# Performance work log

Measured on AMD Instinct MI355X. Metric: run time of the kernel, lower is better.

Reference implementation:

```python
import jax, jax.numpy as jnp
import numpy as np

D_MODEL, D_K, D_V = 1024, 64, 64
B, S = 4, 4096


def setup_inputs() -> dict:
    key = jax.random.key(0)
    ks = jax.random.split(key, 13)
    s = 1.0 / np.sqrt(D_MODEL)
    inp = {
        "q": jax.random.normal(ks[0], (B, S, D_MODEL), jnp.float32),
        "k": jax.random.normal(ks[1], (B, S, D_MODEL), jnp.float32),
        "v": jax.random.normal(ks[2], (B, S, D_MODEL), jnp.float32),
        "mask": jax.random.randint(ks[3], (1, S, S), 0, 2, jnp.int32),
        "Wq": jax.random.normal(ks[4], (D_K, D_MODEL), jnp.float32) * s,
        "bq": jax.random.normal(ks[5], (D_K,), jnp.float32) * s,
        "Wk": jax.random.normal(ks[6], (D_K, D_MODEL), jnp.float32) * s,
        "bk": jax.random.normal(ks[7], (D_K,), jnp.float32) * s,
        "Wv": jax.random.normal(ks[8], (D_V, D_MODEL), jnp.float32) * s,
        "bv": jax.random.normal(ks[9], (D_V,), jnp.float32) * s,
        "Wo": jax.random.normal(ks[10], (D_MODEL, D_V), jnp.float32) / np.sqrt(D_V),
        "bo": jax.random.normal(ks[11], (D_MODEL,), jnp.float32) / np.sqrt(D_V),
    }
    return inp


def reference(q, k, v, mask, Wq, bq, Wk, bk, Wv, bv, Wo, bo):
    # linear projections (torch Linear: x @ W.T + b)
    qh = jnp.einsum("bsd,kd->bsk", q, Wq) + bq   # [B,S,d_k]
    kh = jnp.einsum("bsd,kd->bsk", k, Wk) + bk   # [B,S,d_k]
    vh = jnp.einsum("bsd,vd->bsv", v, Wv) + bv   # [B,S,d_v]
    scale = 1.0 / jnp.sqrt(jnp.float32(D_K))
    scores = jnp.einsum("bqk,bmk->bqm", qh, kh) * scale  # [B,S,S]
    scores = jnp.where(mask == 0, jnp.float32(-1e9), scores)
    attn = jax.nn.softmax(scores, axis=-1)
    out = jnp.einsum("bqm,bmv->bqv", attn, vh)   # [B,S,d_v]
    return jnp.einsum("bqv,dv->bqd", out, Wo) + bo
```

## Files before the change

### kernel.cpp

```cpp
#include <hip/hip_runtime.h>
#include <cmath>

typedef __attribute__((ext_vector_type(8))) short bf16x8;
typedef __attribute__((ext_vector_type(4))) short bf16x4;
typedef __attribute__((ext_vector_type(4))) float f32x4;
typedef unsigned int u32;
typedef __attribute__((address_space(1))) const u32 gu32;
typedef __attribute__((address_space(3))) u32 lu32;

constexpr int B_ = 4;
constexpr int S_ = 4096;
constexpr int DM_ = 1024;
constexpr int DK_ = 64;
constexpr int NROW = B_ * S_;

__device__ __forceinline__ short f2bf(float x) {
  union { float f; unsigned u; } c; c.f = x;
  unsigned r = (c.u + 0x7FFF + ((c.u >> 16) & 1)) >> 16;
  return (short)r;
}
__device__ __forceinline__ float bf2f(short h) {
  union { float f; unsigned u; } c; c.u = ((unsigned)(unsigned short)h) << 16;
  return c.f;
}
__device__ __forceinline__ void gl16(const void* g, void* l) {
  __builtin_amdgcn_global_load_lds((gu32*)g, (lu32*)l, 16, 0, 0);
}

__global__ __launch_bounds__(256) void prep(
    const int* __restrict__ mask, unsigned long long* __restrict__ bits,
    const float* __restrict__ Wq, const float* __restrict__ Wk,
    const float* __restrict__ Wv, short* __restrict__ wbf) {
  if (blockIdx.x < 1024) {
    const int wid = (blockIdx.x * 256 + threadIdx.x) >> 6;
    const int lane = threadIdx.x & 63;
    const size_t base = (size_t)wid * 4096;
    for (int it = 0; it < 64; ++it) {
      int m = mask[base + it * 64 + lane];
      unsigned long long b = __ballot(m != 0);
      if (lane == 0) bits[(size_t)wid * 64 + it] = b;
    }
  } else {
    const int mat = blockIdx.x - 1024;
    const float* W = mat == 0 ? Wq : (mat == 1 ? Wk : Wv);
    short* dst = wbf + (size_t)mat * DK_ * DM_;
    const int t = threadIdx.x;
#pragma unroll 4
    for (int i = 0; i < 32; ++i) {
      int idx = i * 2048 + t * 8;
      f32x4 a0 = *(const f32x4*)(W + idx);
      f32x4 a1 = *(const f32x4*)(W + idx + 4);
      bf16x8 h;
#pragma unroll
      for (int j = 0; j < 4; ++j) { h[j] = f2bf(a0[j]); h[j + 4] = f2bf(a1[j]); }
      *(bf16x8*)(dst + idx) = h;
    }
  }
}

__global__ __launch_bounds__(256) void proj_mfma(
    const float* __restrict__ q, const float* __restrict__ k,
    const float* __restrict__ v, const short* __restrict__ wbf,
    const float* __restrict__ bq, const float* __restrict__ bk,
    const float* __restrict__ bv,
    short* __restrict__ qh, short* __restrict__ kh, short* __restrict__ vhT) {
  __shared__ __align__(16) char smem[49152];

  const int mat = blockIdx.z;
  const char* Xb = (const char*)(mat == 0 ? q : (mat == 1 ? k : v));
  const char* Wb = (const char*)(wbf + (size_t)mat * DK_ * DM_);
  const float* bias = mat == 0 ? bq : (mat == 1 ? bk : bv);

  const int t = threadIdx.x;
  const int row0 = blockIdx.x * 64;
  const int lane = t & 63, w = t >> 6, quad = lane >> 4, l16 = lane & 15;

  f32x4 acc[4] = {};

  auto stage = [&](int buf, int ks) {
    const int k0 = ks * 64;
#pragma unroll
    for (int i = 0; i < 4; ++i) {
      int o = t * 16 + i * 4096;
      int row = o >> 8, col = o & 255;
      int scol = col ^ ((row & 7) << 4);
      gl16(Xb + (size_t)(row0 + row) * (DM_ * 4) + k0 * 4 + scol,
           smem + buf * 16384 + o);
    }
#pragma unroll
    for (int i = 0; i < 2; ++i) {
      int o = t * 16 + i * 4096;
      int row = o >> 7, col = o & 127;
      int scol = col ^ ((row & 7) << 4);
      gl16(Wb + row * 2048 + k0 * 2 + scol,
           smem + 32768 + buf * 8192 + o);
    }
  };

  auto compute = [&](int buf) {
    const char* xs = smem + buf * 16384;
    const char* ws = smem + 32768 + buf * 8192;
    const int xrow = 16 * w + l16;
    const int xsw = (xrow & 7) << 4;
#pragma unroll
    for (int c = 0; c < 2; ++c) {
      bf16x8 bw[4];
#pragma unroll
      for (int ct = 0; ct < 4; ++ct) {
        int wr = 16 * ct + l16;
        bw[ct] = *(const bf16x8*)(ws + wr * 128 +
                                  ((c * 64 + quad * 16) ^ ((wr & 7) << 4)));
      }
      int xb = xrow * 256 + ((c * 128 + quad * 32) ^ xsw);
      f32x4 x0 = *(const f32x4*)(xs + xb);
      f32x4 x1 = *(const f32x4*)(xs + (xb ^ 16));
      bf16x8 ahi, alo;
#pragma unroll
      for (int j = 0; j < 4; ++j) {
        short h0 = f2bf(x0[j]); ahi[j] = h0;     alo[j]     = f2bf(x0[j] - bf2f(h0));
        short h1 = f2bf(x1[j]); ahi[j + 4] = h1; alo[j + 4] = f2bf(x1[j] - bf2f(h1));
      }
#pragma unroll
      for (int ct = 0; ct < 4; ++ct) {
        acc[ct] = __builtin_amdgcn_mfma_f32_16x16x32_bf16(ahi, bw[ct], acc[ct], 0, 0, 0);
        acc[ct] = __builtin_amdgcn_mfma_f32_16x16x32_bf16(alo, bw[ct], acc[ct], 0, 0, 0);
      }
    }
  };

  stage(0, 0);
  __syncthreads();
  int cur = 0;
#pragma unroll 1
  for (int ks = 0; ks < 16; ++ks) {
    if (ks < 15) stage(cur ^ 1, ks + 1);
    compute(cur);
    __syncthreads();
    cur ^= 1;
  }

  float bs[4];
#pragma unroll
  for (int ct = 0; ct < 4; ++ct) bs[ct] = bias[16 * ct + l16];

  short* dstq = (mat == 0) ? qh : kh;
#pragma unroll
  for (int ct = 0; ct < 4; ++ct)
#pragma unroll
    for (int reg = 0; reg < 4; ++reg) {
      int r = row0 + 16 * w + quad * 4 + reg;
      int c = 16 * ct + l16;
      short hv = f2bf(acc[ct][reg] + bs[ct]);
      if (mat == 2)
        vhT[((size_t)(r >> 12) * DK_ + c) * S_ + (r & 4095)] = hv;
      else
        dstq[(size_t)r * DK_ + c] = hv;
    }
}

__global__ __launch_bounds__(256) void attn_mfma(
    const short* __restrict__ qh, const short* __restrict__ kh,
    const short* __restrict__ vhT, const unsigned int* __restrict__ mbits,
    float* __restrict__ Opart, float* __restrict__ mpart,
    float* __restrict__ lpart, int ns) {
  __shared__ short ks[64][72];
  __shared__ short vt[64][72];
  __shared__ short ps[4][16][72];

  const int b = blockIdx.z;
  const int split = blockIdx.y;
  const int q0 = blockIdx.x * 64;
  const int t = threadIdx.x, lane = t & 63, w = t >> 6;
  const int quad = lane >> 4, l16 = lane & 15;
  const int myq = q0 + 16 * w + l16;

  const int kt0 = split * (S_ / ns);
  const int kt1 = kt0 + S_ / ns;

  bf16x8 qf[2];
  {
    const short* src = qh + ((size_t)b * S_ + myq) * DK_ + quad * 8;
    qf[0] = *(const bf16x8*)src;
    qf[1] = *(const bf16x8*)(src + 32);
  }

  f32x4 ao[4] = {};
  float m_i = -INFINITY, l_i = 0.0f;

  const int sr = t >> 2;
  const int sseg = t & 3;

  for (int kt = kt0; kt < kt1; kt += 64) {
    __syncthreads();
    {
      const short* srck = kh + ((size_t)b * S_ + kt + sr) * DK_;
      *(bf16x8*)&ks[sr][8 * sseg]       = *(const bf16x8*)(srck + 8 * sseg);
      *(bf16x8*)&ks[sr][8 * (sseg + 4)] = *(const bf16x8*)(srck + 8 * (sseg + 4));
      const short* srcv = vhT + ((size_t)b * DK_ + sr) * S_ + kt;
      *(bf16x8*)&vt[sr][8 * sseg]       = *(const bf16x8*)(srcv + 8 * sseg);
      *(bf16x8*)&vt[sr][8 * (sseg + 4)] = *(const bf16x8*)(srcv + 8 * (sseg + 4));
    }
    const uint2 mw = *(const uint2*)&mbits[(size_t)myq * 128 + (kt >> 5)];
    __syncthreads();

    f32x4 sacc[4] = {};
#pragma unroll
    for (int c = 0; c < 2; ++c)
#pragma unroll
      for (int tt = 0; tt < 4; ++tt) {
        bf16x8 a = *(const bf16x8*)&ks[16 * tt + l16][c * 32 + quad * 8];
        sacc[tt] = __builtin_amdgcn_mfma_f32_16x16x32_bf16(a, qf[c], sacc[tt], 0, 0, 0);
      }

    float sc[16];
#pragma unroll
    for (int tt = 0; tt < 4; ++tt) {
      unsigned wrd = (tt & 2) ? mw.y : mw.x;
      int base = (tt & 1) * 16 + quad * 4;
#pragma unroll
      for (int r = 0; r < 4; ++r)
        sc[tt * 4 + r] = ((wrd >> (base + r)) & 1) ? sacc[tt][r] * 0.125f : -1e9f;
    }

    float mx = sc[0];
#pragma unroll
    for (int i = 1; i < 16; ++i) mx = fmaxf(mx, sc[i]);
    mx = fmaxf(mx, __shfl_xor(mx, 16));
    mx = fmaxf(mx, __shfl_xor(mx, 32));
    float m_new = fmaxf(m_i, mx);
    float alpha = __expf(m_i - m_new);
    float p[16], sum = 0.0f;
#pragma unroll
    for (int i = 0; i < 16; ++i) { p[i] = __expf(sc[i] - m_new); sum += p[i]; }
    sum += __shfl_xor(sum, 16);
    sum += __shfl_xor(sum, 32);
    l_i = l_i * alpha + sum;
    m_i = m_new;

#pragma unroll
    for (int tt = 0; tt < 4; ++tt) {
      bf16x4 pk;
#pragma unroll
      for (int r = 0; r < 4; ++r) pk[r] = f2bf(p[tt * 4 + r]);
      *(bf16x4*)&ps[w][l16][16 * tt + quad * 4] = pk;
    }

#pragma unroll
    for (int dt = 0; dt < 4; ++dt)
#pragma unroll
      for (int r = 0; r < 4; ++r) ao[dt][r] *= alpha;

#pragma unroll
    for (int c = 0; c < 2; ++c) {
      bf16x8 bp = *(const bf16x8*)&ps[w][l16][c * 32 + quad * 8];
#pragma unroll
      for (int dt = 0; dt < 4; ++dt) {
        bf16x8 av = *(const bf16x8*)&vt[16 * dt + l16][c * 32 + quad * 8];
        ao[dt] = __builtin_amdgcn_mfma_f32_16x16x32_bf16(av, bp, ao[dt], 0, 0, 0);
      }
    }
  }

  const size_t prow = (size_t)split * NROW + (size_t)b * S_ + myq;
#pragma unroll
  for (int dt = 0; dt < 4; ++dt)
    *(f32x4*)&Opart[prow * DK_ + 16 * dt + quad * 4] = ao[dt];
  if (quad == 0) {
    mpart[prow] = m_i;
    lpart[prow] = l_i;
  }
}

__global__ __launch_bounds__(256) void attn_combine(
    const float* __restrict__ Opart, const float* __restrict__ mpart,
    const float* __restrict__ lpart, short* __restrict__ o_bf, int ns) {
  const int t = threadIdx.x;
  const int row = blockIdx.x * 64 + (t >> 2);
  const int c0 = (t & 3) * 16;

  float M = -INFINITY;
  for (int s = 0; s < ns; ++s) M = fmaxf(M, mpart[(size_t)s * NROW + row]);
  float L = 0.0f, wt[4];
  for (int s = 0; s < ns; ++s) {
    wt[s] = __expf(mpart[(size_t)s * NROW + row] - M);
    L += wt[s] * lpart[(size_t)s * NROW + row];
  }
  float acc[16] = {};
  for (int s = 0; s < ns; ++s) {
    const float* src = Opart + ((size_t)s * NROW + row) * DK_ + c0;
#pragma unroll
    for (int j = 0; j < 16; j += 4) {
      f32x4 vv = *(const f32x4*)(src + j);
#pragma unroll
      for (int r = 0; r < 4; ++r) acc[j + r] += wt[s] * vv[r];
    }
  }
  const float inv = 1.0f / L;
  bf16x8 o0, o1;
#pragma unroll
  for (int j = 0; j < 8; ++j) {
    o0[j] = f2bf(acc[j] * inv);
    o1[j] = f2bf(acc[j + 8] * inv);
  }
  *(bf16x8*)&o_bf[(size_t)row * DK_ + c0]     = o0;
  *(bf16x8*)&o_bf[(size_t)row * DK_ + c0 + 8] = o1;
}

__global__ __launch_bounds__(256) void outproj_mfma(
    const short* __restrict__ o_bf, const float* __restrict__ Wo,
    const float* __restrict__ bo, float* __restrict__ out) {
  __shared__ short os[64][72];
  __shared__ short wos[256][72];

  const int t = threadIdx.x, lane = t & 63, w = t >> 6;
  const int quad = lane >> 4, l16 = lane & 15;
  const int s0 = blockIdx.y * 64;
  const int dm0 = blockIdx.x * 256;

  {
    int r = t >> 2, cq = (t & 3) * 16;
    const short* src = o_bf + (size_t)(s0 + r) * DK_ + cq;
    *(bf16x8*)&os[r][cq]     = *(const bf16x8*)src;
    *(bf16x8*)&os[r][cq + 8] = *(const bf16x8*)(src + 8);
  }
#pragma unroll
  for (int pass = 0; pass < 4; ++pass) {
    int r = pass * 64 + (t >> 2), cq = (t & 3) * 16;
    const float* src = Wo + (size_t)(dm0 + r) * DK_ + cq;
    f32x4 a0 = *(const f32x4*)src, a1 = *(const f32x4*)(src + 4);
    f32x4 a2 = *(const f32x4*)(src + 8), a3 = *(const f32x4*)(src + 12);
    bf16x8 v0, v1;
#pragma unroll
    for (int j = 0; j < 4; ++j) {
      v0[j] = f2bf(a0[j]); v0[j + 4] = f2bf(a1[j]);
      v1[j] = f2bf(a2[j]); v1[j + 4] = f2bf(a3[j]);
    }
    *(bf16x8*)&wos[r][cq]     = v0;
    *(bf16x8*)&wos[r][cq + 8] = v1;
  }
  __syncthreads();

  bf16x8 af[2];
#pragma unroll
  for (int c = 0; c < 2; ++c)
    af[c] = *(const bf16x8*)&os[16 * w + l16][c * 32 + quad * 8];

  f32x4 acc[16] = {};
#pragma unroll
  for (int c = 0; c < 2; ++c)
#pragma unroll
    for (int nt = 0; nt < 16; ++nt) {
      bf16x8 bw = *(const bf16x8*)&wos[16 * nt + l16][c * 32 + quad * 8];
      acc[nt] = __builtin_amdgcn_mfma_f32_16x16x32_bf16(af[c], bw, acc[nt], 0, 0, 0);
    }

  float bias_r[16];
#pragma unroll
  for (int nt = 0; nt < 16; ++nt) bias_r[nt] = bo[dm0 + 16 * nt + l16];

#pragma unroll
  for (int nt = 0; nt < 16; ++nt)
#pragma unroll
    for (int reg = 0; reg < 4; ++reg) {
      int s = s0 + 16 * w + quad * 4 + reg;
      int dm = dm0 + 16 * nt + l16;
      out[(size_t)s * DM_ + dm] = acc[nt][reg] + bias_r[nt];
    }
}

extern "C" void kernel_launch(void* const* d_in, const int* in_sizes, int n_in,
                              void* d_out, int out_size, void* d_ws,
                              size_t ws_size, hipStream_t stream) {
  (void)in_sizes; (void)n_in; (void)out_size;
  const float* q  = (const float*)d_in[0];
  const float* k  = (const float*)d_in[1];
  const float* v  = (const float*)d_in[2];
  const int* mask = (const int*)d_in[3];
  const float* Wq = (const float*)d_in[4];
  const float* bq = (const float*)d_in[5];
  const float* Wk = (const float*)d_in[6];
  const float* bk = (const float*)d_in[7];
  const float* Wv = (const float*)d_in[8];
  const float* bv = (const float*)d_in[9];
  const float* Wo = (const float*)d_in[10];
  const float* bo = (const float*)d_in[11];
  float* out = (float*)d_out;

  short* qh  = (short*)d_ws;
  short* kh  = qh + (size_t)NROW * DK_;
  short* vhT = kh + (size_t)NROW * DK_;
  unsigned int* mbits = (unsigned int*)(vhT + (size_t)NROW * DK_);
  short* o_bf = (short*)(mbits + (size_t)S_ * 128);
  float* mpart = (float*)(o_bf + (size_t)NROW * DK_);
  float* lpart = mpart + 4 * NROW;
  float* Opart = lpart + 4 * NROW;
  short* wbf = (short*)Opart;

  const size_t base_bytes = (size_t)((char*)Opart - (char*)d_ws);
  const size_t per_split = (size_t)NROW * DK_ * sizeof(float);
  int ns = 1;
  if (ws_size >= base_bytes + 4 * per_split) ns = 4;
  else if (ws_size >= base_bytes + 2 * per_split) ns = 2;

  prep<<<1027, 256, 0, stream>>>(mask, (unsigned long long*)mbits,
                                 Wq, Wk, Wv, wbf);
  proj_mfma<<<dim3(NROW / 64, 1, 3), 256, 0, stream>>>(
      q, k, v, wbf, bq, bk, bv, qh, kh, vhT);
  attn_mfma<<<dim3(S_ / 64, ns, B_), 256, 0, stream>>>(
      qh, kh, vhT, mbits, Opart, mpart, lpart, ns);
  attn_combine<<<NROW / 64, 256, 0, stream>>>(Opart, mpart, lpart, o_bf, ns);
  outproj_mfma<<<dim3(DM_ / 256, NROW / 64), 256, 0, stream>>>(o_bf, Wo, bo, out);
}
```

Before: 380.3 us.

## Load projection operands directly into registers instead of LDS staging

The projection kernel drops its double-buffered LDS staging with async global-to-LDS copies and barriers. Each lane now loads its own X row slice straight into registers, prefetching the next k-step, and reads bf16 weight fragments directly from global memory. This is meant to remove LDS traffic and __syncthreads overhead, since X rows are not shared across waves. In exchange, weight fragments are re-read from cache by every wave, and there is less latency hiding than a shared buffered pipeline gives.

New measurement: 382.8 us. No clear change (+0.7%).

```diff
diff --git a/kernel.cpp b/kernel.cpp
--- a/kernel.cpp
+++ b/kernel.cpp
@@ -4,9 +4,6 @@
 typedef __attribute__((ext_vector_type(8))) short bf16x8;
 typedef __attribute__((ext_vector_type(4))) short bf16x4;
 typedef __attribute__((ext_vector_type(4))) float f32x4;
-typedef unsigned int u32;
-typedef __attribute__((address_space(1))) const u32 gu32;
-typedef __attribute__((address_space(3))) u32 lu32;
 
 constexpr int B_ = 4;
 constexpr int S_ = 4096;
@@ -22,9 +19,6 @@
 __device__ __forceinline__ float bf2f(short h) {
   union { float f; unsigned u; } c; c.u = ((unsigned)(unsigned short)h) << 16;
   return c.f;
-}
-__device__ __forceinline__ void gl16(const void* g, void* l) {
-  __builtin_amdgcn_global_load_lds((gu32*)g, (lu32*)l, 16, 0, 0);
 }
 
 __global__ __launch_bounds__(256) void prep(
@@ -64,56 +58,51 @@
     const float* __restrict__ bq, const float* __restrict__ bk,
     const float* __restrict__ bv,
     short* __restrict__ qh, short* __restrict__ kh, short* __restrict__ vhT) {
-  __shared__ __align__(16) char smem[49152];
-
   const int mat = blockIdx.z;
-  const char* Xb = (const char*)(mat == 0 ? q : (mat == 1 ? k : v));
-  const char* Wb = (const char*)(wbf + (size_t)mat * DK_ * DM_);
+  const float* X    = mat == 0 ? q : (mat == 1 ? k : v);
+  const short* W    = wbf + (size_t)mat * DK_ * DM_;
   const float* bias = mat == 0 ? bq : (mat == 1 ? bk : bv);
 
   const int t = threadIdx.x;
   const int row0 = blockIdx.x * 64;
   const int lane = t & 63, w = t >> 6, quad = lane >> 4, l16 = lane & 15;
 
+  const int myrow = row0 + 16 * w + l16;
+  const float* xp = X + (size_t)myrow * DM_ + quad * 8;
+  const short* wp = W + (size_t)l16 * DM_ + quad * 8;
+
   f32x4 acc[4] = {};
 
-  auto stage = [&](int buf, int ks) {
-    const int k0 = ks * 64;
-#pragma unroll
-    for (int i = 0; i < 4; ++i) {
-      int o = t * 16 + i * 4096;
-      int row = o >> 8, col = o & 255;
-      int scol = col ^ ((row & 7) << 4);
-      gl16(Xb + (size_t)(row0 + row) * (DM_ * 4) + k0 * 4 + scol,
-           smem + buf * 16384 + o);
-    }
-#pragma unroll
-    for (int i = 0; i < 2; ++i) {
-      int o = t * 16 + i * 4096;
-      int row = o >> 7, col = o & 127;
-      int scol = col ^ ((row & 7) << 4);
-      gl16(Wb + row * 2048 + k0 * 2 + scol,
-           smem + 32768 + buf * 8192 + o);
-    }
-  };
-
-  auto compute = [&](int buf) {
-    const char* xs = smem + buf * 16384;
-    const char* ws = smem + 32768 + buf * 8192;
-    const int xrow = 16 * w + l16;
-    const int xsw = (xrow & 7) << 4;
+  f32x4 xc0, xc1, xc2, xc3;
+  f32x4 xn0, xn1, xn2, xn3;
+
+  xc0 = *(const f32x4*)(xp + 0);
+  xc1 = *(const f32x4*)(xp + 4);
+  xc2 = *(const f32x4*)(xp + 32);
+  xc3 = *(const f32x4*)(xp + 36);
+
+#pragma unroll 1
+  for (int ks = 0; ks < 16; ++ks) {
+    if (ks < 15) {
+      const float* xq = xp + (ks + 1) * 64;
+      xn0 = *(const f32x4*)(xq + 0);
+      xn1 = *(const f32x4*)(xq + 4);
+      xn2 = *(const f32x4*)(xq + 32);
+      xn3 = *(const f32x4*)(xq + 36);
+    }
+
+    bf16x8 wf[2][4];
+#pragma unroll
+    for (int c = 0; c < 2; ++c)
+#pragma unroll
+      for (int ct = 0; ct < 4; ++ct)
+        wf[c][ct] = *(const bf16x8*)(wp + (size_t)ct * (16 * DM_) +
+                                     ks * 64 + c * 32);
+
 #pragma unroll
     for (int c = 0; c < 2; ++c) {
-      bf16x8 bw[4];
-#pragma unroll
-      for (int ct = 0; ct < 4; ++ct) {
-        int wr = 16 * ct + l16;
-        bw[ct] = *(const bf16x8*)(ws + wr * 128 +
-                                  ((c * 64 + quad * 16) ^ ((wr & 7) << 4)));
-      }
-      int xb = xrow * 256 + ((c * 128 + quad * 32) ^ xsw);
-      f32x4 x0 = *(const f32x4*)(xs + xb);
-      f32x4 x1 = *(const f32x4*)(xs + (xb ^ 16));
+      f32x4 x0 = (c == 0) ? xc0 : xc2;
+      f32x4 x1 = (c == 0) ? xc1 : xc3;
       bf16x8 ahi, alo;
 #pragma unroll
       for (int j = 0; j < 4; ++j) {
@@ -122,21 +111,12 @@
       }
 #pragma unroll
       for (int ct = 0; ct < 4; ++ct) {
-        acc[ct] = __builtin_amdgcn_mfma_f32_16x16x32_bf16(ahi, bw[ct], acc[ct], 0, 0, 0);
-        acc[ct] = __builtin_amdgcn_mfma_f32_16x16x32_bf16(alo, bw[ct], acc[ct], 0, 0, 0);
+        acc[ct] = __builtin_amdgcn_mfma_f32_16x16x32_bf16(ahi, wf[c][ct], acc[ct], 0, 0, 0);
+        acc[ct] = __builtin_amdgcn_mfma_f32_16x16x32_bf16(alo, wf[c][ct], acc[ct], 0, 0, 0);
       }
     }
-  };
-
-  stage(0, 0);
-  __syncthreads();
-  int cur = 0;
-#pragma unroll 1
-  for (int ks = 0; ks < 16; ++ks) {
-    if (ks < 15) stage(cur ^ 1, ks + 1);
-    compute(cur);
-    __syncthreads();
-    cur ^= 1;
+
+    xc0 = xn0; xc1 = xn1; xc2 = xn2; xc3 = xn3;
   }
 
   float bs[4];
```
